# Kernel tuning notes

Hardware: AMD Instinct MI355X
Metric: run time of the kernel (lower is better)

Reference implementation:

```python
import jax, jax.numpy as jnp
import numpy as np

V = 20000; FV = 2000; PV = 31
SE = 400; FE = 50; PE = 5; NE = 5
FR = FE + PE + NE  # 60, field_rep_embed_size
H = 512; HH = H // 2  # decoder hidden, encoder per-direction hidden
B = 32; T = 32; S = 100
TE = 300  # target_lookup dim (hardcoded in module)


def setup_inputs() -> dict:
    key = jax.random.key(0)
    ks = jax.random.split(key, 26)
    g = lambda k, shape, s: (jax.random.normal(k, shape, jnp.float32) * s)
    inp = {}
    inp['sent'] = jax.random.randint(ks[0], (B, T), 0, V)
    inp['value'] = jax.random.randint(ks[1], (B, S), 0, V)
    inp['field'] = jax.random.randint(ks[2], (B, S), 0, FV)
    inp['ppos'] = jax.random.randint(ks[3], (B, S), 0, PV)
    inp['pneg'] = jax.random.randint(ks[4], (B, S), 0, PV)
    inp['batch_size'] = B
    inp['value_mask'] = jnp.ones((B, S), jnp.float32)
    inp['align_prob'] = jax.random.uniform(ks[5], (B, S, V), jnp.float32)
    # embedding tables
    inp['sent_emb'] = g(ks[6], (V, SE), 0.05)
    inp['field_emb'] = g(ks[7], (FV, FE), 0.05)
    inp['ppos_emb'] = g(ks[8], (PV, PE), 0.05)
    inp['pneg_emb'] = g(ks[9], (PV, NE), 0.05)
    inp['target_emb'] = g(ks[10], (V, TE), 0.05)
    # bidirectional encoder LSTM (per-direction hidden HH), torch gate order i,f,g,o
    ein = SE + FR
    inp['Wi_f'] = g(ks[11], (ein, 4 * HH), ein ** -0.5)
    inp['Wh_f'] = g(ks[12], (HH, 4 * HH), HH ** -0.5)
    inp['b_f'] = jnp.zeros((4 * HH,), jnp.float32)
    inp['Wi_b'] = g(ks[13], (ein, 4 * HH), ein ** -0.5)
    inp['Wh_b'] = g(ks[14], (HH, 4 * HH), HH ** -0.5)
    inp['b_b'] = jnp.zeros((4 * HH,), jnp.float32)
    # decoder LSTM cell + dual attention params
    inp['Wi_d'] = g(ks[15], (SE, 4 * H), SE ** -0.5)
    inp['Wh_d'] = g(ks[16], (H, 4 * H), H ** -0.5)
    inp['b_d'] = jnp.zeros((4 * H,), jnp.float32)
    inp['Wa'] = g(ks[17], (H, H), H ** -0.5)   # encoder-state attention proj
    inp['Wf'] = g(ks[18], (FR, H), FR ** -0.5) # field-rep attention proj
    inp['Wo'] = g(ks[19], (2 * H, H), (2 * H) ** -0.5)  # output proj [h;ctx]
    inp['Wl'] = g(ks[20], (2 * H + SE, 1), (2 * H + SE) ** -0.5)  # lamda gate
    inp['bl'] = jnp.zeros((1,), jnp.float32)
    # linear_out: encoder_hidden_size -> vocab
    inp['Wout'] = g(ks[21], (H, V), H ** -0.5)
    inp['bout'] = jnp.zeros((V,), jnp.float32)
    return inp


def _cell(x, h, c, Wi, Wh, b):
    z = x @ Wi + h @ Wh + b
    i, f, g, o = jnp.split(z, 4, axis=-1)
    c = jax.nn.sigmoid(f) * c + jax.nn.sigmoid(i) * jnp.tanh(g)
    h = jax.nn.sigmoid(o) * jnp.tanh(c)
    return h, c


def _run_lstm(xseq, Wi, Wh, b):
    # xseq [B,L,E] -> hs [B,L,Hn], (hT, cT)
    Bn = xseq.shape[0]; Hn = Wh.shape[0]
    init = (jnp.zeros((Bn, Hn), xseq.dtype), jnp.zeros((Bn, Hn), xseq.dtype))
    def step(carry, xt):
        h, c = _cell(xt, carry[0], carry[1], Wi, Wh, b)
        return (h, c), h
    (hT, cT), hs = jax.lax.scan(step, init, jnp.swapaxes(xseq, 0, 1))
    return jnp.swapaxes(hs, 0, 1), hT, cT


def reference(sent, value, field, ppos, pneg, batch_size, value_mask, align_prob,
              sent_emb, field_emb, ppos_emb, pneg_emb, target_emb,
              Wi_f, Wh_f, b_f, Wi_b, Wh_b, b_b,
              Wi_d, Wh_d, b_d, Wa, Wf, Wo, Wl, bl, Wout, bout):
    # --- encoder input: word emb of table values + field/pos/neg-pos embs ---
    input_d = sent_emb[value]                                     # [B,S,SE]
    input_z = jnp.concatenate([field_emb[field], ppos_emb[ppos], pneg_emb[pneg]], axis=2)  # [B,S,FR]
    enc_in = jnp.concatenate([input_d, input_z], axis=2)          # [B,S,SE+FR]
    # bidirectional LSTM (dropout is eval-mode identity)
    hs_f, hTf, cTf = _run_lstm(enc_in, Wi_f, Wh_f, b_f)
    hs_b, hTb, cTb = _run_lstm(enc_in[:, ::-1], Wi_b, Wh_b, b_b)
    enc_out = jnp.concatenate([hs_f, hs_b[:, ::-1]], axis=-1)     # [B,S,H]
    h0 = jnp.concatenate([hTf, hTb], axis=-1)                     # [B,H]
    c0 = jnp.concatenate([cTf, cTb], axis=-1)

    # --- dual-attention decoder ---
    x_seq = sent_emb[sent]                                        # [B,T,SE]
    enc_proj = jnp.einsum('bsh,hk->bsk', enc_out, Wa)             # word-level keys
    z_proj = jnp.einsum('bsf,fk->bsk', input_z, Wf)               # field-level keys

    def dstep(carry, xt):
        h, c = _cell(xt, carry[0], carry[1], Wi_d, Wh_d, b_d)
        alpha = jax.nn.softmax(jnp.einsum('bsh,bh->bs', enc_proj, h), axis=-1)
        beta = jax.nn.softmax(jnp.einsum('bsh,bh->bs', z_proj, h), axis=-1)
        g = alpha * beta
        g = g / (jnp.sum(g, axis=-1, keepdims=True) + 1e-9)       # dual attn weights
        ctx = jnp.einsum('bs,bsh->bh', g, enc_out)
        out = jnp.tanh(jnp.concatenate([h, ctx], axis=-1) @ Wo)   # [B,H]
        lam = jax.nn.sigmoid(jnp.concatenate([h, ctx, xt], axis=-1) @ Wl + bl)  # [B,1]
        return (h, c), (out, g, lam)

    (hT, cT), (outs, attn, lam) = jax.lax.scan(dstep, (h0, c0), jnp.swapaxes(x_seq, 0, 1))
    outs = jnp.swapaxes(outs, 0, 1)   # [B,T,H]
    attn = jnp.swapaxes(attn, 0, 1)   # [B,T,S]
    lam = jnp.swapaxes(lam, 0, 1)     # [B,T,1]

    p_mod = jax.nn.log_softmax(outs @ Wout + bout, axis=2)        # [B,T,V]
    p_lex = jnp.einsum('bts,bsv->btv', attn, align_prob)          # bmm
    p_bias = jax.nn.log_softmax(lam * p_lex + (1.0 - lam) * p_mod, axis=2)

    # position_idx_to_value: vectorized gather replacing the scalar double loop
    max_idx_attn = jnp.argmax(attn, axis=2)                       # [B,T]
    word_idx = jnp.take_along_axis(value, max_idx_attn, axis=1)   # [B,T]
    attn_pred = target_emb[word_idx]                              # [B,T,300]
    decoder_pred = target_emb[jnp.argmax(p_bias, axis=2)]         # [B,T,300]
    return p_bias, (hT, cT), attn_pred, decoder_pred
```

## Files before the change

### kernel.cpp

```cpp
#include <hip/hip_runtime.h>
#include <cstdint>
#include <cstddef>

static constexpr int Bn  = 32;
static constexpr int Tn  = 32;
static constexpr int Sn  = 100;
static constexpr int Vn  = 20000;
static constexpr int SEn = 400;
static constexpr int EINn= 460;
static constexpr int Hn  = 512;
static constexpr int HHn = 256;
static constexpr int TEn = 300;

__device__ __forceinline__ float sigm(float x) { return 1.f / (1.f + expf(-x)); }

__device__ __forceinline__ void fma4(float hk, const float4 w,
                                     float& zi, float& zf, float& zg, float& zo) {
    zi = fmaf(hk, w.x, zi); zf = fmaf(hk, w.y, zf);
    zg = fmaf(hk, w.z, zg); zo = fmaf(hk, w.w, zo);
}

__global__ __launch_bounds__(256) void embed_kernel(
    const int* __restrict__ value, const int* __restrict__ field,
    const int* __restrict__ ppos, const int* __restrict__ pneg,
    const int* __restrict__ sent,
    const float* __restrict__ sent_emb, const float* __restrict__ field_emb,
    const float* __restrict__ ppos_emb, const float* __restrict__ pneg_emb,
    float* __restrict__ enc_in, float* __restrict__ x_seq)
{
    int i = blockIdx.x * 256 + threadIdx.x;
    const int total1 = Bn * Sn * EINn;
    if (i < total1) {
        int e = i % EINn, bs = i / EINn;
        float v;
        if (e < SEn)      v = sent_emb[(size_t)value[bs] * SEn + e];
        else if (e < 450) v = field_emb[field[bs] * 50 + (e - 400)];
        else if (e < 455) v = ppos_emb[ppos[bs] * 5 + (e - 450)];
        else              v = pneg_emb[pneg[bs] * 5 + (e - 455)];
        enc_in[i] = v;
    } else {
        int i2 = i - total1;
        if (i2 < Bn * Tn * SEn) {
            int e = i2 % SEn, bt = i2 / SEn;
            x_seq[i2] = sent_emb[(size_t)sent[bt] * SEn + e];
        }
    }
}

__global__ __launch_bounds__(256) void transpose_wh_kernel(
    const float* __restrict__ Whf, const float* __restrict__ Whb,
    const float* __restrict__ Whd,
    float* __restrict__ Whf_t, float* __restrict__ Whb_t, float* __restrict__ Whd_t)
{
    int i = blockIdx.x * 256 + threadIdx.x;
    if (i < 65536) {
        int k = i >> 8, u = i & 255;
        const float* p = Whf + (size_t)k * 1024 + u;
        float4 o;
        o.x = p[0]; o.y = p[256]; o.z = p[512]; o.w = p[768];
        *(float4*)(Whf_t + (size_t)i * 4) = o;
        p = Whb + (size_t)k * 1024 + u;
        o.x = p[0]; o.y = p[256]; o.z = p[512]; o.w = p[768];
        *(float4*)(Whb_t + (size_t)i * 4) = o;
    } else {
        int j = i - 65536;
        if (j < 262144) {
            int k = j >> 9, u = j & 511;
            const float* p = Whd + (size_t)k * 2048 + u;
            float4 o;
            o.x = p[0]; o.y = p[512]; o.z = p[1024]; o.w = p[1536];
            *(float4*)(Whd_t + (size_t)j * 4) = o;
        }
    }
}

__global__ __launch_bounds__(256) void gemm128_kernel(
    const float* __restrict__ A, const float* __restrict__ Bm,
    const float* __restrict__ bias, float* __restrict__ C,
    int M, int N, int K, int lda, int ldb, int ldc)
{
    __shared__ float As[8][128];
    __shared__ float Bs[8][128];
    const int bm = blockIdx.y * 128, bn = blockIdx.x * 128;
    const int tid = threadIdx.x;
    const int tx = tid & 15, ty = tid >> 4;
    const int row0 = ty * 8, col0 = tx * 8;
    float acc[8][8] = {};
    for (int k0 = 0; k0 < K; k0 += 8) {
        #pragma unroll
        for (int i = 0; i < 4; ++i) {
            int idx = tid + 256 * i;
            int m = idx >> 3, kk = idx & 7;
            float v = 0.f;
            if (bm + m < M && k0 + kk < K) v = A[(size_t)(bm + m) * lda + (k0 + kk)];
            As[kk][m] = v;
        }
        #pragma unroll
        for (int i = 0; i < 4; ++i) {
            int idx = tid + 256 * i;
            int kk = idx >> 7, n = idx & 127;
            float v = 0.f;
            if (k0 + kk < K && bn + n < N) v = Bm[(size_t)(k0 + kk) * ldb + (bn + n)];
            Bs[kk][n] = v;
        }
        __syncthreads();
        #pragma unroll
        for (int kk = 0; kk < 8; ++kk) {
            float a[8], b[8];
            #pragma unroll
            for (int i = 0; i < 8; ++i) a[i] = As[kk][row0 + i];
            #pragma unroll
            for (int j = 0; j < 8; ++j) b[j] = Bs[kk][col0 + j];
            #pragma unroll
            for (int i = 0; i < 8; ++i)
                #pragma unroll
                for (int j = 0; j < 8; ++j) acc[i][j] = fmaf(a[i], b[j], acc[i][j]);
        }
        __syncthreads();
    }
    #pragma unroll
    for (int i = 0; i < 8; ++i) {
        int m = bm + row0 + i;
        if (m >= M) continue;
        #pragma unroll
        for (int j = 0; j < 8; ++j) {
            int n = bn + col0 + j;
            if (n < N) {
                float v = acc[i][j];
                if (bias) v += bias[n];
                C[(size_t)m * ldc + n] = v;
            }
        }
    }
}

__global__ __launch_bounds__(256) void enc_lstm2_kernel(
    const float* __restrict__ Xf, const float* __restrict__ Xb,
    const float4* __restrict__ Whf_t, const float4* __restrict__ Whb_t,
    float* __restrict__ enc_out, float* __restrict__ h0, float* __restrict__ c0)
{
    const int b = blockIdx.x >> 1, dir = blockIdx.x & 1;
    const float* __restrict__ X = dir ? Xb : Xf;
    const float4* __restrict__ W = dir ? Whb_t : Whf_t;
    __shared__ __align__(16) float h_sh[HHn];
    const int u = threadIdx.x;
    float c = 0.f;
    h_sh[u] = 0.f;
    __syncthreads();
    for (int step = 0; step < Sn; ++step) {
        const int s = dir ? (Sn - 1 - step) : step;
        const float* xr = X + ((size_t)(b * Sn + s)) * 1024;
        float zi = xr[u], zf = xr[256 + u], zg = xr[512 + u], zo = xr[768 + u];
        #pragma unroll 4
        for (int k4 = 0; k4 < 64; ++k4) {
            const float4 hv = *(const float4*)&h_sh[k4 << 2];
            const float4 w0 = W[((k4 << 2) + 0) * 256 + u];
            const float4 w1 = W[((k4 << 2) + 1) * 256 + u];
            const float4 w2 = W[((k4 << 2) + 2) * 256 + u];
            const float4 w3 = W[((k4 << 2) + 3) * 256 + u];
            fma4(hv.x, w0, zi, zf, zg, zo);
            fma4(hv.y, w1, zi, zf, zg, zo);
            fma4(hv.z, w2, zi, zf, zg, zo);
            fma4(hv.w, w3, zi, zf, zg, zo);
        }
        c = sigm(zf) * c + sigm(zi) * tanhf(zg);
        float h = sigm(zo) * tanhf(c);
        __syncthreads();
        h_sh[u] = h;
        enc_out[((size_t)(b * Sn + s)) * Hn + dir * HHn + u] = h;
        if (step == Sn - 1) {
            h0[b * Hn + dir * HHn + u] = h;
            c0[b * Hn + dir * HHn + u] = c;
        }
        __syncthreads();
    }
}

__global__ __launch_bounds__(256) void dec_lstm2_kernel(
    const float* __restrict__ Xd, const float4* __restrict__ Whd_t,
    const float* __restrict__ h0, const float* __restrict__ c0,
    float* __restrict__ h_all, float* __restrict__ hT, float* __restrict__ cT,
    float* __restrict__ hbuf, int* __restrict__ bar)
{
    const int b = blockIdx.x >> 1;
    const int tid = threadIdx.x;
    const int u = ((blockIdx.x & 1) << 8) + tid;
    __shared__ __align__(16) float h_sh[Hn];
    h_sh[tid]       = h0[b * Hn + tid];
    h_sh[tid + 256] = h0[b * Hn + 256 + tid];
    float c = c0[b * Hn + u];
    __syncthreads();
    for (int t = 0; t < Tn; ++t) {
        const float* xr = Xd + ((size_t)(b * Tn + t)) * 2048;
        float zi = xr[u], zf = xr[512 + u], zg = xr[1024 + u], zo = xr[1536 + u];
        #pragma unroll 4
        for (int k4 = 0; k4 < 128; ++k4) {
            const float4 hv = *(const float4*)&h_sh[k4 << 2];
            const float4 w0 = Whd_t[((k4 << 2) + 0) * 512 + u];
            const float4 w1 = Whd_t[((k4 << 2) + 1) * 512 + u];
            const float4 w2 = Whd_t[((k4 << 2) + 2) * 512 + u];
            const float4 w3 = Whd_t[((k4 << 2) + 3) * 512 + u];
            fma4(hv.x, w0, zi, zf, zg, zo);
            fma4(hv.y, w1, zi, zf, zg, zo);
            fma4(hv.z, w2, zi, zf, zg, zo);
            fma4(hv.w, w3, zi, zf, zg, zo);
        }
        c = sigm(zf) * c + sigm(zi) * tanhf(zg);
        float h = sigm(zo) * tanhf(c);
        h_all[((size_t)(b * Tn + t)) * Hn + u] = h;
        if (t == Tn - 1) { hT[b * Hn + u] = h; cT[b * Hn + u] = c; }
        __hip_atomic_store(&hbuf[b * Hn + u], h, __ATOMIC_RELEASE, __HIP_MEMORY_SCOPE_AGENT);
        __syncthreads();
        if (t == Tn - 1) break;
        if (tid == 0) {
            __hip_atomic_fetch_add(bar, 1, __ATOMIC_ACQ_REL, __HIP_MEMORY_SCOPE_AGENT);
            const int target = 64 * (t + 1);
            while (__hip_atomic_load(bar, __ATOMIC_ACQUIRE, __HIP_MEMORY_SCOPE_AGENT) < target)
                __builtin_amdgcn_s_sleep(8);
        }
        __syncthreads();
        h_sh[tid]       = __hip_atomic_load(&hbuf[b * Hn + tid],       __ATOMIC_ACQUIRE, __HIP_MEMORY_SCOPE_AGENT);
        h_sh[tid + 256] = __hip_atomic_load(&hbuf[b * Hn + 256 + tid], __ATOMIC_ACQUIRE, __HIP_MEMORY_SCOPE_AGENT);
        __syncthreads();
    }
}

__global__ __launch_bounds__(256) void dec_post_kernel(
    const float* __restrict__ h_all, const float* __restrict__ enc_proj,
    const float* __restrict__ z_proj, const float* __restrict__ enc_out,
    const float* __restrict__ x_seq, const float* __restrict__ Wo,
    const float* __restrict__ Wl, const float* __restrict__ bl,
    const int* __restrict__ value, const float* __restrict__ target_emb,
    float* __restrict__ outs, float* __restrict__ gattn,
    float* __restrict__ lamv, float* __restrict__ attn_pred)
{
    const int bt = blockIdx.x, b = bt >> 5;
    const int tid = threadIdx.x;
    __shared__ float h_sh[Hn];
    __shared__ float sc[2 * Sn];
    __shared__ float g_sh[Sn];
    __shared__ float ctx_sh[Hn];
    __shared__ float red[256];
    __shared__ int smax_sh;

    for (int i = tid; i < Hn; i += 256) h_sh[i] = h_all[(size_t)bt * Hn + i];
    __syncthreads();

    const int wave = tid >> 6, lane = tid & 63;
    for (int s = wave; s < Sn; s += 4) {
        const float* ep = enc_proj + ((size_t)b * Sn + s) * Hn;
        const float* zp = z_proj  + ((size_t)b * Sn + s) * Hn;
        float da = 0.f, db = 0.f;
        for (int j = lane; j < Hn; j += 64) {
            float hv = h_sh[j];
            da = fmaf(ep[j], hv, da);
            db = fmaf(zp[j], hv, db);
        }
        #pragma unroll
        for (int off = 32; off; off >>= 1) {
            da += __shfl_down(da, off);
            db += __shfl_down(db, off);
        }
        if (lane == 0) { sc[s] = da; sc[Sn + s] = db; }
    }
    __syncthreads();

    if (tid == 0) {
        float ma = -1e30f, mb = -1e30f;
        for (int s = 0; s < Sn; ++s) { ma = fmaxf(ma, sc[s]); mb = fmaxf(mb, sc[Sn + s]); }
        float sa = 0.f, sb = 0.f;
        for (int s = 0; s < Sn; ++s) {
            float ea = expf(sc[s] - ma), eb = expf(sc[Sn + s] - mb);
            sc[s] = ea; sc[Sn + s] = eb; sa += ea; sb += eb;
        }
        float gs = 0.f;
        for (int s = 0; s < Sn; ++s) { float g = (sc[s] / sa) * (sc[Sn + s] / sb); g_sh[s] = g; gs += g; }
        float inv = 1.f / (gs + 1e-9f);
        float best = -1.f; int bi = 0;
        for (int s = 0; s < Sn; ++s) {
            float g = g_sh[s] * inv; g_sh[s] = g;
            if (g > best) { best = g; bi = s; }
        }
        smax_sh = bi;
    }
    __syncthreads();

    for (int s = tid; s < Sn; s += 256) gattn[(size_t)bt * Sn + s] = g_sh[s];
    const int word = value[b * Sn + smax_sh];
    for (int e = tid; e < TEn; e += 256)
        attn_pred[(size_t)bt * TEn + e] = target_emb[(size_t)word * TEn + e];

    for (int u = tid; u < Hn; u += 256) {
        float acc = 0.f;
        for (int s = 0; s < Sn; ++s)
            acc = fmaf(g_sh[s], enc_out[((size_t)b * Sn + s) * Hn + u], acc);
        ctx_sh[u] = acc;
    }
    __syncthreads();

    for (int j = tid; j < Hn; j += 256) {
        float acc = 0.f;
        for (int k = 0; k < Hn; ++k) acc = fmaf(h_sh[k], Wo[(size_t)k * Hn + j], acc);
        for (int k = 0; k < Hn; ++k) acc = fmaf(ctx_sh[k], Wo[(size_t)(Hn + k) * Hn + j], acc);
        outs[(size_t)bt * Hn + j] = tanhf(acc);
    }

    float part = 0.f;
    for (int k = tid; k < Hn; k += 256) part = fmaf(h_sh[k], Wl[k], part);
    for (int k = tid; k < Hn; k += 256) part = fmaf(ctx_sh[k], Wl[Hn + k], part);
    const float* xr = x_seq + (size_t)bt * SEn;
    for (int k = tid; k < SEn; k += 256) part = fmaf(xr[k], Wl[2 * Hn + k], part);
    red[tid] = part;
    __syncthreads();
    for (int s2 = 128; s2; s2 >>= 1) {
        if (tid < s2) red[tid] += red[tid + s2];
        __syncthreads();
    }
    if (tid == 0) lamv[bt] = 1.f / (1.f + expf(-(red[0] + bl[0])));
}

__global__ __launch_bounds__(256) void p_lex_kernel(
    const float* __restrict__ gattn, const float* __restrict__ align_prob,
    float* __restrict__ p_lex)
{
    const int b = blockIdx.z, th = blockIdx.y, vc = blockIdx.x;
    const int tid = threadIdx.x;
    __shared__ float gT[Sn][17];
    for (int i = tid; i < Sn * 16; i += 256) {
        int s = i >> 4, tt = i & 15;
        gT[s][tt] = gattn[((size_t)(b * Tn + th * 16 + tt)) * Sn + s];
    }
    __syncthreads();
    const int v0 = vc * 1024 + tid * 4;
    if (v0 >= Vn) return;
    float acc[16][4] = {};
    for (int s = 0; s < Sn; ++s) {
        const float4 a = *(const float4*)(align_prob + ((size_t)b * Sn + s) * Vn + v0);
        #pragma unroll
        for (int tt = 0; tt < 16; ++tt) {
            float g = gT[s][tt];
            acc[tt][0] = fmaf(g, a.x, acc[tt][0]);
            acc[tt][1] = fmaf(g, a.y, acc[tt][1]);
            acc[tt][2] = fmaf(g, a.z, acc[tt][2]);
            acc[tt][3] = fmaf(g, a.w, acc[tt][3]);
        }
    }
    #pragma unroll
    for (int tt = 0; tt < 16; ++tt) {
        float4 o;
        o.x = acc[tt][0]; o.y = acc[tt][1]; o.z = acc[tt][2]; o.w = acc[tt][3];
        *(float4*)(p_lex + ((size_t)(b * Tn + th * 16 + tt)) * Vn + v0) = o;
    }
}

__global__ __launch_bounds__(256) void reduce1_kernel(
    const float* __restrict__ z, float* __restrict__ lse1)
{
    const int r = blockIdx.x, tid = threadIdx.x;
    const float* row = z + (size_t)r * Vn;
    __shared__ float red[256];
    float m = -1e30f;
    for (int v = tid; v < Vn; v += 256) m = fmaxf(m, row[v]);
    red[tid] = m; __syncthreads();
    for (int s = 128; s; s >>= 1) { if (tid < s) red[tid] = fmaxf(red[tid], red[tid + s]); __syncthreads(); }
    m = red[0]; __syncthreads();
    float sum = 0.f;
    for (int v = tid; v < Vn; v += 256) sum += expf(row[v] - m);
    red[tid] = sum; __syncthreads();
    for (int s = 128; s; s >>= 1) { if (tid < s) red[tid] += red[tid + s]; __syncthreads(); }
    if (tid == 0) lse1[r] = m + logf(red[0]);
}

__global__ __launch_bounds__(256) void combine_kernel(
    float* __restrict__ q, const float* __restrict__ p_lex,
    const float* __restrict__ lamv, const float* __restrict__ lse1,
    float* __restrict__ lse2, int* __restrict__ amax)
{
    const int r = blockIdx.x, tid = threadIdx.x;
    const float l = lamv[r], ls1 = lse1[r];
    float* row = q + (size_t)r * Vn;
    const float* pl = p_lex + (size_t)r * Vn;
    __shared__ float rm[256];
    __shared__ int ri[256];
    float m = -1e30f; int mi = 0;
    for (int v = tid; v < Vn; v += 256) {
        float qq = l * pl[v] + (1.f - l) * (row[v] - ls1);
        row[v] = qq;
        if (qq > m) { m = qq; mi = v; }
    }
    rm[tid] = m; ri[tid] = mi; __syncthreads();
    for (int s = 128; s; s >>= 1) {
        if (tid < s) {
            if (rm[tid + s] > rm[tid] || (rm[tid + s] == rm[tid] && ri[tid + s] < ri[tid])) {
                rm[tid] = rm[tid + s]; ri[tid] = ri[tid + s];
            }
        }
        __syncthreads();
    }
    m = rm[0];
    const int best = ri[0];
    __syncthreads();
    float sum = 0.f;
    for (int v = tid; v < Vn; v += 256) sum += expf(row[v] - m);
    rm[tid] = sum; __syncthreads();
    for (int s = 128; s; s >>= 1) { if (tid < s) rm[tid] += rm[tid + s]; __syncthreads(); }
    if (tid == 0) { lse2[r] = m + logf(rm[0]); amax[r] = best; }
}

__global__ __launch_bounds__(256) void finalize_kernel(
    float* __restrict__ pbias, const float* __restrict__ lse2,
    const int* __restrict__ amax, const float* __restrict__ target_emb,
    float* __restrict__ dec_pred)
{
    const int r = blockIdx.x, tid = threadIdx.x;
    const float ls = lse2[r];
    float* row = pbias + (size_t)r * Vn;
    for (int v = tid; v < Vn; v += 256) row[v] -= ls;
    const int wd = amax[r];
    for (int e = tid; e < TEn; e += 256)
        dec_pred[(size_t)r * TEn + e] = target_emb[(size_t)wd * TEn + e];
}

extern "C" void kernel_launch(void* const* d_in, const int* in_sizes, int n_in,
                              void* d_out, int out_size, void* d_ws, size_t ws_size,
                              hipStream_t stream)
{
    const int*   sent       = (const int*)d_in[0];
    const int*   value      = (const int*)d_in[1];
    const int*   field      = (const int*)d_in[2];
    const int*   ppos       = (const int*)d_in[3];
    const int*   pneg       = (const int*)d_in[4];
    const float* align_prob = (const float*)d_in[7];
    const float* sent_emb   = (const float*)d_in[8];
    const float* field_emb  = (const float*)d_in[9];
    const float* ppos_emb   = (const float*)d_in[10];
    const float* pneg_emb   = (const float*)d_in[11];
    const float* target_emb = (const float*)d_in[12];
    const float* Wi_f = (const float*)d_in[13];
    const float* Wh_f = (const float*)d_in[14];
    const float* b_f  = (const float*)d_in[15];
    const float* Wi_b = (const float*)d_in[16];
    const float* Wh_b = (const float*)d_in[17];
    const float* b_b  = (const float*)d_in[18];
    const float* Wi_d = (const float*)d_in[19];
    const float* Wh_d = (const float*)d_in[20];
    const float* b_d  = (const float*)d_in[21];
    const float* Wa   = (const float*)d_in[22];
    const float* Wf   = (const float*)d_in[23];
    const float* Wo   = (const float*)d_in[24];
    const float* Wl   = (const float*)d_in[25];
    const float* bl   = (const float*)d_in[26];
    const float* Wout = (const float*)d_in[27];
    const float* bout = (const float*)d_in[28];

    float* w = (float*)d_ws;
    float* enc_in   = w; w += (size_t)Bn * Sn * EINn;
    float* x_seq    = w; w += (size_t)Bn * Tn * SEn;
    float* Xf       = w; w += (size_t)Bn * Sn * 1024;
    float* Xb       = w; w += (size_t)Bn * Sn * 1024;
    float* Xd       = w; w += (size_t)Bn * Tn * 2048;
    float* enc_out  = w; w += (size_t)Bn * Sn * Hn;
    float* enc_proj = w; w += (size_t)Bn * Sn * Hn;
    float* z_proj   = w; w += (size_t)Bn * Sn * Hn;
    float* h0       = w; w += (size_t)Bn * Hn;
    float* c0       = w; w += (size_t)Bn * Hn;
    float* h_all    = w; w += (size_t)Bn * Tn * Hn;
    float* outs     = w; w += (size_t)Bn * Tn * Hn;
    float* gattn    = w; w += (size_t)Bn * Tn * Sn;
    float* lamv     = w; w += (size_t)Bn * Tn;
    float* p_lex    = w; w += (size_t)Bn * Tn * Vn;
    float* lse1     = w; w += (size_t)Bn * Tn;
    float* lse2     = w; w += (size_t)Bn * Tn;
    int*   amax     = (int*)w;

    float* Whf_t = p_lex;
    float* Whb_t = p_lex + 262144;
    float* Whd_t = p_lex + 524288;
    float* hbuf  = p_lex + 2000000;
    int*   bar   = (int*)(p_lex + 2100000);

    float* outp      = (float*)d_out;
    float* pbias     = outp;
    float* hT        = outp + (size_t)20480000;
    float* cT        = hT + Bn * Hn;
    float* attn_pred = cT + Bn * Hn;
    float* dec_pred  = attn_pred + (size_t)Bn * Tn * TEn;

    embed_kernel<<<7350, 256, 0, stream>>>(value, field, ppos, pneg, sent,
        sent_emb, field_emb, ppos_emb, pneg_emb, enc_in, x_seq);
    transpose_wh_kernel<<<1280, 256, 0, stream>>>(Wh_f, Wh_b, Wh_d, Whf_t, Whb_t, Whd_t);

    dim3 gXf(8, 25);
    gemm128_kernel<<<gXf, 256, 0, stream>>>(enc_in, Wi_f, b_f, Xf, 3200, 1024, 460, 460, 1024, 1024);
    gemm128_kernel<<<gXf, 256, 0, stream>>>(enc_in, Wi_b, b_b, Xb, 3200, 1024, 460, 460, 1024, 1024);
    dim3 gXd(16, 8);
    gemm128_kernel<<<gXd, 256, 0, stream>>>(x_seq, Wi_d, b_d, Xd, 1024, 2048, 400, 400, 2048, 2048);

    enc_lstm2_kernel<<<64, 256, 0, stream>>>(Xf, Xb, (const float4*)Whf_t,
        (const float4*)Whb_t, enc_out, h0, c0);

    dim3 gPr(4, 25);
    gemm128_kernel<<<gPr, 256, 0, stream>>>(enc_out, Wa, nullptr, enc_proj, 3200, 512, 512, 512, 512, 512);
    gemm128_kernel<<<gPr, 256, 0, stream>>>(enc_in + 400, Wf, nullptr, z_proj, 3200, 512, 60, 460, 512, 512);

    hipMemsetAsync(bar, 0, 64, stream);
    {
        void* args[] = { (void*)&Xd, (void*)&Whd_t, (void*)&h0, (void*)&c0,
                         (void*)&h_all, (void*)&hT, (void*)&cT,
                         (void*)&hbuf, (void*)&bar };
        hipLaunchCooperativeKernel((const void*)dec_lstm2_kernel,
                                   dim3(64), dim3(256), args, 0, stream);
    }

    dec_post_kernel<<<1024, 256, 0, stream>>>(h_all, enc_proj, z_proj, enc_out, x_seq,
        Wo, Wl, bl, value, target_emb, outs, gattn, lamv, attn_pred);

    dim3 gBig(157, 8);
    gemm128_kernel<<<gBig, 256, 0, stream>>>(outs, Wout, bout, pbias, 1024, 20000, 512, 512, 20000, 20000);

    dim3 gPl(20, 2, 32);
    p_lex_kernel<<<gPl, 256, 0, stream>>>(gattn, align_prob, p_lex);

    reduce1_kernel<<<1024, 256, 0, stream>>>(pbias, lse1);
    combine_kernel<<<1024, 256, 0, stream>>>(pbias, p_lex, lamv, lse1, lse2, amax);
    finalize_kernel<<<1024, 256, 0, stream>>>(pbias, lse2, amax, target_emb, dec_pred);

    (void)in_sizes; (void)n_in; (void)out_size; (void)ws_size;
}
```

Baseline: 4.200 ms.

## Split LSTM recurrences across more blocks with per-sequence flag sync and K-split

The encoder and decoder LSTM recurrences move from 64 blocks to 256 cooperative blocks. Each block owns 64 hidden units and splits the K reduction across four wavefronts, summing the partials in shared memory. Hidden state is exchanged through global memory, with per-sequence atomic flags replacing the single global barrier, and the recurrent weights are relaid out per unit slice so reads coalesce. This spreads the serial per-step matvec over more CUs and shrinks barrier scope. The cost is a global flag spin plus a hidden-state reload on every step.

```diff
diff --git a/kernel.cpp b/kernel.cpp
--- a/kernel.cpp
+++ b/kernel.cpp
@@ -13,12 +13,6 @@
 static constexpr int TEn = 300;
 
 __device__ __forceinline__ float sigm(float x) { return 1.f / (1.f + expf(-x)); }
-
-__device__ __forceinline__ void fma4(float hk, const float4 w,
-                                     float& zi, float& zf, float& zg, float& zo) {
-    zi = fmaf(hk, w.x, zi); zf = fmaf(hk, w.y, zf);
-    zg = fmaf(hk, w.z, zg); zo = fmaf(hk, w.w, zo);
-}
 
 __global__ __launch_bounds__(256) void embed_kernel(
     const int* __restrict__ value, const int* __restrict__ field,
@@ -50,26 +44,30 @@
 __global__ __launch_bounds__(256) void transpose_wh_kernel(
     const float* __restrict__ Whf, const float* __restrict__ Whb,
     const float* __restrict__ Whd,
-    float* __restrict__ Whf_t, float* __restrict__ Whb_t, float* __restrict__ Whd_t)
+    float4* __restrict__ Whf_t, float4* __restrict__ Whb_t, float4* __restrict__ Whd_t)
 {
     int i = blockIdx.x * 256 + threadIdx.x;
     if (i < 65536) {
         int k = i >> 8, u = i & 255;
+        int q = u >> 6, ul = u & 63;
+        size_t oidx = ((size_t)(q * 256 + k)) * 64 + ul;
         const float* p = Whf + (size_t)k * 1024 + u;
         float4 o;
         o.x = p[0]; o.y = p[256]; o.z = p[512]; o.w = p[768];
-        *(float4*)(Whf_t + (size_t)i * 4) = o;
+        Whf_t[oidx] = o;
         p = Whb + (size_t)k * 1024 + u;
         o.x = p[0]; o.y = p[256]; o.z = p[512]; o.w = p[768];
-        *(float4*)(Whb_t + (size_t)i * 4) = o;
+        Whb_t[oidx] = o;
     } else {
-        int j = i - 65536;
-        if (j < 262144) {
-            int k = j >> 9, u = j & 511;
+        int j0 = i - 65536;
+        if (j0 < 262144) {
+            int k = j0 >> 9, u = j0 & 511;
+            int jj = u >> 6, ul = u & 63;
+            size_t oidx = ((size_t)(jj * 512 + k)) * 64 + ul;
             const float* p = Whd + (size_t)k * 2048 + u;
             float4 o;
             o.x = p[0]; o.y = p[512]; o.z = p[1024]; o.w = p[1536];
-            *(float4*)(Whd_t + (size_t)j * 4) = o;
+            Whd_t[oidx] = o;
         }
     }
 }
@@ -134,93 +132,133 @@
     }
 }
 
-__global__ __launch_bounds__(256) void enc_lstm2_kernel(
+__global__ __launch_bounds__(256) void enc_lstm3_kernel(
     const float* __restrict__ Xf, const float* __restrict__ Xb,
     const float4* __restrict__ Whf_t, const float4* __restrict__ Whb_t,
-    float* __restrict__ enc_out, float* __restrict__ h0, float* __restrict__ c0)
-{
-    const int b = blockIdx.x >> 1, dir = blockIdx.x & 1;
+    float* __restrict__ enc_out, float* __restrict__ h0, float* __restrict__ c0,
+    float* __restrict__ hbufE, int* __restrict__ flagE)
+{
+    const int id = blockIdx.x;
+    const int b = id >> 3, dir = (id >> 2) & 1, q = id & 3;
+    const int U0 = q * 64;
+    const int tid = threadIdx.x;
+    const int u = tid & 63, kq = tid >> 6;
+    const int k0 = kq * 64;
     const float* __restrict__ X = dir ? Xb : Xf;
     const float4* __restrict__ W = dir ? Whb_t : Whf_t;
+    const int grp = b * 2 + dir;
+    float* __restrict__ hx = hbufE + grp * HHn;
+    int* __restrict__ flg = flagE + grp * 16;
+
     __shared__ __align__(16) float h_sh[HHn];
-    const int u = threadIdx.x;
+    __shared__ float4 part[4][64];
+
+    h_sh[tid] = 0.f;
     float c = 0.f;
-    h_sh[u] = 0.f;
-    __syncthreads();
+    __syncthreads();
+
     for (int step = 0; step < Sn; ++step) {
         const int s = dir ? (Sn - 1 - step) : step;
-        const float* xr = X + ((size_t)(b * Sn + s)) * 1024;
-        float zi = xr[u], zf = xr[256 + u], zg = xr[512 + u], zo = xr[768 + u];
+        float4 z = make_float4(0.f, 0.f, 0.f, 0.f);
+        const float4* wp = W + ((size_t)(q * 256 + k0)) * 64 + u;
         #pragma unroll 4
-        for (int k4 = 0; k4 < 64; ++k4) {
-            const float4 hv = *(const float4*)&h_sh[k4 << 2];
-            const float4 w0 = W[((k4 << 2) + 0) * 256 + u];
-            const float4 w1 = W[((k4 << 2) + 1) * 256 + u];
-            const float4 w2 = W[((k4 << 2) + 2) * 256 + u];
-            const float4 w3 = W[((k4 << 2) + 3) * 256 + u];
-            fma4(hv.x, w0, zi, zf, zg, zo);
-            fma4(hv.y, w1, zi, zf, zg, zo);
-            fma4(hv.z, w2, zi, zf, zg, zo);
-            fma4(hv.w, w3, zi, zf, zg, zo);
-        }
-        c = sigm(zf) * c + sigm(zi) * tanhf(zg);
-        float h = sigm(zo) * tanhf(c);
-        __syncthreads();
-        h_sh[u] = h;
-        enc_out[((size_t)(b * Sn + s)) * Hn + dir * HHn + u] = h;
-        if (step == Sn - 1) {
-            h0[b * Hn + dir * HHn + u] = h;
-            c0[b * Hn + dir * HHn + u] = c;
-        }
-        __syncthreads();
-    }
-}
-
-__global__ __launch_bounds__(256) void dec_lstm2_kernel(
+        for (int k = 0; k < 64; ++k) {
+            const float hk = h_sh[k0 + k];
+            const float4 w = wp[(size_t)k * 64];
+            z.x = fmaf(hk, w.x, z.x); z.y = fmaf(hk, w.y, z.y);
+            z.z = fmaf(hk, w.z, z.z); z.w = fmaf(hk, w.w, z.w);
+        }
+        part[kq][u] = z;
+        __syncthreads();
+        if (tid < 64) {
+            float4 z0 = part[0][tid], z1 = part[1][tid], z2 = part[2][tid], z3 = part[3][tid];
+            const float* xr = X + ((size_t)(b * Sn + s)) * 1024;
+            float zi = z0.x + z1.x + z2.x + z3.x + xr[U0 + tid];
+            float zf = z0.y + z1.y + z2.y + z3.y + xr[256 + U0 + tid];
+            float zg = z0.z + z1.z + z2.z + z3.z + xr[512 + U0 + tid];
+            float zo = z0.w + z1.w + z2.w + z3.w + xr[768 + U0 + tid];
+            c = sigm(zf) * c + sigm(zi) * tanhf(zg);
+            float h = sigm(zo) * tanhf(c);
+            enc_out[((size_t)(b * Sn + s)) * Hn + dir * HHn + U0 + tid] = h;
+            if (step == Sn - 1) {
+                h0[b * Hn + dir * HHn + U0 + tid] = h;
+                c0[b * Hn + dir * HHn + U0 + tid] = c;
+            }
+            __hip_atomic_store(&hx[U0 + tid], h, __ATOMIC_RELEASE, __HIP_MEMORY_SCOPE_AGENT);
+        }
+        __syncthreads();
+        if (step == Sn - 1) break;
+        if (tid == 0) {
+            __hip_atomic_fetch_add(flg, 1, __ATOMIC_ACQ_REL, __HIP_MEMORY_SCOPE_AGENT);
+            const int target = 4 * (step + 1);
+            while (__hip_atomic_load(flg, __ATOMIC_ACQUIRE, __HIP_MEMORY_SCOPE_AGENT) < target)
+                __builtin_amdgcn_s_sleep(2);
+        }
+        __syncthreads();
+        h_sh[tid] = __hip_atomic_load(&hx[tid], __ATOMIC_ACQUIRE, __HIP_MEMORY_SCOPE_AGENT);
+        __syncthreads();
+    }
+}
+
+__global__ __launch_bounds__(256) void dec_lstm3_kernel(
     const float* __restrict__ Xd, const float4* __restrict__ Whd_t,
     const float* __restrict__ h0, const float* __restrict__ c0,
     float* __restrict__ h_all, float* __restrict__ hT, float* __restrict__ cT,
-    float* __restrict__ hbuf, int* __restrict__ bar)
-{
-    const int b = blockIdx.x >> 1;
+    float* __restrict__ hbufD, int* __restrict__ flagD)
+{
+    const int id = blockIdx.x;
+    const int b = id >> 3, j = id & 7;
+    const int U0 = j * 64;
     const int tid = threadIdx.x;
-    const int u = ((blockIdx.x & 1) << 8) + tid;
+    const int u = tid & 63, kq = tid >> 6;
+    const int k0 = kq * 128;
+    float* __restrict__ hx = hbufD + b * Hn;
+    int* __restrict__ flg = flagD + b * 16;
+
     __shared__ __align__(16) float h_sh[Hn];
+    __shared__ float4 part[4][64];
+
     h_sh[tid]       = h0[b * Hn + tid];
     h_sh[tid + 256] = h0[b * Hn + 256 + tid];
-    float c = c0[b * Hn + u];
-    __syncthreads();
+    float c = (tid < 64) ? c0[b * Hn + U0 + tid] : 0.f;
+    __syncthreads();
+
     for (int t = 0; t < Tn; ++t) {
-        const float* xr = Xd + ((size_t)(b * Tn + t)) * 2048;
-        float zi = xr[u], zf = xr[512 + u], zg = xr[1024 + u], zo = xr[1536 + u];
+        float4 z = make_float4(0.f, 0.f, 0.f, 0.f);
+        const float4* wp = Whd_t + ((size_t)(j * 512 + k0)) * 64 + u;
         #pragma unroll 4
-        for (int k4 = 0; k4 < 128; ++k4) {
-            const float4 hv = *(const float4*)&h_sh[k4 << 2];
-            const float4 w0 = Whd_t[((k4 << 2) + 0) * 512 + u];
-            const float4 w1 = Whd_t[((k4 << 2) + 1) * 512 + u];
-            const float4 w2 = Whd_t[((k4 << 2) + 2) * 512 + u];
-            const float4 w3 = Whd_t[((k4 << 2) + 3) * 512 + u];
-            fma4(hv.x, w0, zi, zf, zg, zo);
-            fma4(hv.y, w1, zi, zf, zg, zo);
-            fma4(hv.z, w2, zi, zf, zg, zo);
-            fma4(hv.w, w3, zi, zf, zg, zo);
-        }
-        c = sigm(zf) * c + sigm(zi) * tanhf(zg);
-        float h = sigm(zo) * tanhf(c);
-        h_all[((size_t)(b * Tn + t)) * Hn + u] = h;
-        if (t == Tn - 1) { hT[b * Hn + u] = h; cT[b * Hn + u] = c; }
-        __hip_atomic_store(&hbuf[b * Hn + u], h, __ATOMIC_RELEASE, __HIP_MEMORY_SCOPE_AGENT);
+        for (int k = 0; k < 128; ++k) {
+            const float hk = h_sh[k0 + k];
+            const float4 w = wp[(size_t)k * 64];
+            z.x = fmaf(hk, w.x, z.x); z.y = fmaf(hk, w.y, z.y);
+            z.z = fmaf(hk, w.z, z.z); z.w = fmaf(hk, w.w, z.w);
+        }
+        part[kq][u] = z;
+        __syncthreads();
+        if (tid < 64) {
+            float4 z0 = part[0][tid], z1 = part[1][tid], z2 = part[2][tid], z3 = part[3][tid];
+            const float* xr = Xd + ((size_t)(b * Tn + t)) * 2048;
+            float zi = z0.x + z1.x + z2.x + z3.x + xr[U0 + tid];
+            float zf = z0.y + z1.y + z2.y + z3.y + xr[512 + U0 + tid];
+            float zg = z0.z + z1.z + z2.z + z3.z + xr[1024 + U0 + tid];
+            float zo = z0.w + z1.w + z2.w + z3.w + xr[1536 + U0 + tid];
+            c = sigm(zf) * c + sigm(zi) * tanhf(zg);
+            float h = sigm(zo) * tanhf(c);
+            h_all[((size_t)(b * Tn + t)) * Hn + U0 + tid] = h;
+            if (t == Tn - 1) { hT[b * Hn + U0 + tid] = h; cT[b * Hn + U0 + tid] = c; }
+            __hip_atomic_store(&hx[U0 + tid], h, __ATOMIC_RELEASE, __HIP_MEMORY_SCOPE_AGENT);
+        }
         __syncthreads();
         if (t == Tn - 1) break;
         if (tid == 0) {
-            __hip_atomic_fetch_add(bar, 1, __ATOMIC_ACQ_REL, __HIP_MEMORY_SCOPE_AGENT);
-            const int target = 64 * (t + 1);
-            while (__hip_atomic_load(bar, __ATOMIC_ACQUIRE, __HIP_MEMORY_SCOPE_AGENT) < target)
-                __builtin_amdgcn_s_sleep(8);
-        }
-        __syncthreads();
-        h_sh[tid]       = __hip_atomic_load(&hbuf[b * Hn + tid],       __ATOMIC_ACQUIRE, __HIP_MEMORY_SCOPE_AGENT);
-        h_sh[tid + 256] = __hip_atomic_load(&hbuf[b * Hn + 256 + tid], __ATOMIC_ACQUIRE, __HIP_MEMORY_SCOPE_AGENT);
+            __hip_atomic_fetch_add(flg, 1, __ATOMIC_ACQ_REL, __HIP_MEMORY_SCOPE_AGENT);
+            const int target = 8 * (t + 1);
+            while (__hip_atomic_load(flg, __ATOMIC_ACQUIRE, __HIP_MEMORY_SCOPE_AGENT) < target)
+                __builtin_amdgcn_s_sleep(2);
+        }
+        __syncthreads();
+        h_sh[tid]       = __hip_atomic_load(&hx[tid],       __ATOMIC_ACQUIRE, __HIP_MEMORY_SCOPE_AGENT);
+        h_sh[tid + 256] = __hip_atomic_load(&hx[256 + tid], __ATOMIC_ACQUIRE, __HIP_MEMORY_SCOPE_AGENT);
         __syncthreads();
     }
 }
@@ -476,8 +514,10 @@
     float* Whf_t = p_lex;
     float* Whb_t = p_lex + 262144;
     float* Whd_t = p_lex + 524288;
-    float* hbuf  = p_lex + 2000000;
-    int*   bar   = (int*)(p_lex + 2100000);
+    float* hbufE = p_lex + 2000000;
+    float* hbufD = p_lex + 2020000;
+    int*   flagE = (int*)(p_lex + 2040000);
+    int*   flagD = (int*)(p_lex + 2045000);
 
     float* outp      = (float*)d_out;
     float* pbias     = outp;
@@ -488,7 +528,9 @@
 
     embed_kernel<<<7350, 256, 0, stream>>>(value, field, ppos, pneg, sent,
         sent_emb, field_emb, ppos_emb, pneg_emb, enc_in, x_seq);
-    transpose_wh_kernel<<<1280, 256, 0, stream>>>(Wh_f, Wh_b, Wh_d, Whf_t, Whb_t, Whd_t);
+    transpose_wh_kernel<<<1280, 256, 0, stream>>>(Wh_f, Wh_b, Wh_d,
+        (float4*)Whf_t, (float4*)Whb_t, (float4*)Whd_t);
+    hipMemsetAsync(flagE, 0, 6000 * 4, stream);
 
     dim3 gXf(8, 25);
     gemm128_kernel<<<gXf, 256, 0, stream>>>(enc_in, Wi_f, b_f, Xf, 3200, 1024, 460, 460, 1024, 1024);
@@ -496,20 +538,24 @@
     dim3 gXd(16, 8);
     gemm128_kernel<<<gXd, 256, 0, stream>>>(x_seq, Wi_d, b_d, Xd, 1024, 2048, 400, 400, 2048, 2048);
 
-    enc_lstm2_kernel<<<64, 256, 0, stream>>>(Xf, Xb, (const float4*)Whf_t,
-        (const float4*)Whb_t, enc_out, h0, c0);
+    {
+        void* args[] = { (void*)&Xf, (void*)&Xb, (void*)&Whf_t, (void*)&Whb_t,
+                         (void*)&enc_out, (void*)&h0, (void*)&c0,
+                         (void*)&hbufE, (void*)&flagE };
+        hipLaunchCooperativeKernel((const void*)enc_lstm3_kernel,
+                                   dim3(256), dim3(256), args, 0, stream);
+    }
 
     dim3 gPr(4, 25);
     gemm128_kernel<<<gPr, 256, 0, stream>>>(enc_out, Wa, nullptr, enc_proj, 3200, 512, 512, 512, 512, 512);
     gemm128_kernel<<<gPr, 256, 0, stream>>>(enc_in + 400, Wf, nullptr, z_proj, 3200, 512, 60, 460, 512, 512);
 
-    hipMemsetAsync(bar, 0, 64, stream);
     {
         void* args[] = { (void*)&Xd, (void*)&Whd_t, (void*)&h0, (void*)&c0,
                          (void*)&h_all, (void*)&hT, (void*)&cT,
-                         (void*)&hbuf, (void*)&bar };
-        hipLaunchCooperativeKernel((const void*)dec_lstm2_kernel,
-                                   dim3(64), dim3(256), args, 0, stream);
+                         (void*)&hbufD, (void*)&flagD };
+        hipLaunchCooperativeKernel((const void*)dec_lstm3_kernel,
+                                   dim3(256), dim3(256), args, 0, stream);
     }
 
     dec_post_kernel<<<1024, 256, 0, stream>>>(h_all, enc_proj, z_proj, enc_out, x_seq,
```

Measured after the change: 5.141 ms. 22.4% more time.
